# Performance work log

Hardware: AMD Instinct MI355X
Metric: run time of the kernel (lower is better)

Reference implementation:

```python
import jax, jax.numpy as jnp
import numpy as np

N_NODES = 100000
N_EDGES = 800000
C = 64        # in_channels == out_channels
H = 4         # num_heads
LN_EPS = 1e-5
SM_EPS = 1e-8


def setup_inputs() -> dict:
    key = jax.random.key(0)
    ks = jax.random.split(key, 8)
    return {
        "x": jax.random.normal(ks[0], (N_NODES, C), dtype=jnp.float32),
        "edge_index": jax.random.randint(ks[1], (2, N_EDGES), 0, N_NODES, dtype=jnp.int64),
        "edge_time": jax.random.uniform(ks[2], (N_EDGES,), dtype=jnp.float32),
        "current_time": 1,
        "W_w": jax.random.normal(ks[3], (C, C), dtype=jnp.float32) * (1.0 / np.sqrt(C)),
        "W_b": jnp.zeros((C,), dtype=jnp.float32),
        "attn_w": jax.random.normal(ks[4], (2 * C, H), dtype=jnp.float32) * (1.0 / np.sqrt(2 * C)),
        "attn_b": jnp.zeros((H,), dtype=jnp.float32),
        "decay_rate": jnp.full((1,), 0.1, dtype=jnp.float32),
        "proj_w": jax.random.normal(ks[5], (C * H, C), dtype=jnp.float32) * (1.0 / np.sqrt(C * H)),
        "proj_b": jnp.zeros((C,), dtype=jnp.float32),
        "ln_g": jnp.ones((C,), dtype=jnp.float32),
        "ln_b": jnp.zeros((C,), dtype=jnp.float32),
    }


def reference(x, edge_index, edge_time, current_time, W_w, W_b, attn_w, attn_b,
              decay_rate, proj_w, proj_b, ln_g, ln_b):
    num_nodes = x.shape[0]
    src, dst = edge_index[0], edge_index[1]

    # relation-specific transform (same Linear applied to src and dst node sets)
    h = x @ W_w + W_b                       # (N, C)
    h_src = h[src]                          # (E, C) gather
    h_dst = h[dst]                          # (E, C) gather

    # attention: Linear(2C -> H) + LeakyReLU(0.2)
    logits = h_src @ attn_w[:C] + h_dst @ attn_w[C:] + attn_b   # (E, H)
    scores = jax.nn.leaky_relu(logits, negative_slope=0.2)

    # temporal decay: exp(-softplus(lambda) * delta_t), multiplied pre-softmax
    delta_t = jnp.float32(current_time) - edge_time             # (E,)
    lam = jax.nn.softplus(decay_rate[0])
    scores = scores * jnp.exp(-lam * delta_t)[:, None]

    # segmented (per-destination) softmax over incoming edges
    smax = jax.ops.segment_max(scores, dst, num_segments=num_nodes)   # (N, H)
    e = jnp.exp(scores - smax[dst])                                   # (E, H)
    ssum = jax.ops.segment_sum(e, dst, num_segments=num_nodes)        # (N, H)
    attn = e / (ssum[dst] + SM_EPS)                                   # (E, H)

    # per-edge messages (E, C, H) -> (E, C*H), scatter-add to destinations
    msg = (h_src[:, :, None] * attn[:, None, :]).reshape(-1, C * H)
    agg = jax.ops.segment_sum(msg, dst, num_segments=num_nodes)       # (N, C*H)

    # single edge type -> mean over 1 message is identity
    out = agg @ proj_w + proj_b                                       # (N, C)
    # dropout p=0 (eval) -> identity; residual + LayerNorm + ReLU
    z = out + x
    mu = jnp.mean(z, axis=-1, keepdims=True)
    var = jnp.mean(jnp.square(z - mu), axis=-1, keepdims=True)
    y = ln_g * (z - mu) * jax.lax.rsqrt(var + LN_EPS) + ln_b
    return jax.nn.relu(y)
```

## Files before the change

### kernel.cpp

```cpp
#include <hip/hip_runtime.h>


typedef __attribute__((ext_vector_type(8))) short bf16x8;
typedef __attribute__((ext_vector_type(4))) float f32x4;

__device__ __forceinline__ unsigned short f2bf(float f) {
  unsigned int u = __float_as_uint(f);
  u += 0x7FFFu + ((u >> 16) & 1u);
  return (unsigned short)(u >> 16);
}
__device__ __forceinline__ float bf2f(unsigned short s) {
  return __uint_as_float(((unsigned int)s) << 16);
}

#define FMA4(P, S, R) { P.x = fmaf(S, R.x, P.x); P.y = fmaf(S, R.y, P.y); \
                        P.z = fmaf(S, R.z, P.z); P.w = fmaf(S, R.w, P.w); }

__global__ __launch_bounds__(64) void k_hn(const float* __restrict__ x,
    const float* __restrict__ Ww, const float* __restrict__ Wb,
    const float* __restrict__ attn_w,
    unsigned short* __restrict__ h16, float4* __restrict__ u,
    float4* __restrict__ v, int N)
{
  const int n = blockIdx.x * 64 + threadIdx.x;
  const bool valid = (n < N);
  const int nc = valid ? n : (N - 1);

  float o[64];
  #pragma unroll
  for (int c = 0; c < 64; ++c) o[c] = Wb[c];

  const float* xr = x + (size_t)nc * 64;
  for (int ch = 0; ch < 16; ++ch) {
    float4 xv = *(const float4*)(xr + ch * 4);
    float a[4] = {xv.x, xv.y, xv.z, xv.w};
    #pragma unroll
    for (int kk = 0; kk < 4; ++kk) {
      const float* Wr = Ww + (size_t)(ch * 4 + kk) * 64;
      #pragma unroll
      for (int c = 0; c < 64; ++c)
        o[c] = fmaf(a[kk], Wr[c], o[c]);
    }
  }

  float4 uu = make_float4(0.f, 0.f, 0.f, 0.f);
  float4 vv = make_float4(0.f, 0.f, 0.f, 0.f);
  const float4* aw = (const float4*)attn_w;
  #pragma unroll
  for (int c = 0; c < 64; ++c) {
    float4 r1 = aw[c];
    float4 r2 = aw[64 + c];
    FMA4(uu, o[c], r1);
    FMA4(vv, o[c], r2);
  }

  if (valid) {
    unsigned int* hr = (unsigned int*)(h16 + (size_t)n * 64);
    #pragma unroll
    for (int i = 0; i < 8; ++i) {
      uint4 w;
      w.x = (unsigned int)f2bf(o[i*8+0]) | ((unsigned int)f2bf(o[i*8+1]) << 16);
      w.y = (unsigned int)f2bf(o[i*8+2]) | ((unsigned int)f2bf(o[i*8+3]) << 16);
      w.z = (unsigned int)f2bf(o[i*8+4]) | ((unsigned int)f2bf(o[i*8+5]) << 16);
      w.w = (unsigned int)f2bf(o[i*8+6]) | ((unsigned int)f2bf(o[i*8+7]) << 16);
      *(uint4*)(hr + i * 4) = w;
    }
    u[n] = uu;
    v[n] = vv;
  }
}

__global__ __launch_bounds__(256) void k_score(const float4* __restrict__ u,
    const float4* __restrict__ v,
    const int* __restrict__ ei, const float* __restrict__ et,
    const int* __restrict__ ctime, const float* __restrict__ drate,
    const float* __restrict__ attn_b, float4* __restrict__ est,
    int* __restrict__ deg, int* __restrict__ rank, int E)
{
  int e = blockIdx.x * 256 + threadIdx.x;
  if (e >= E) return;
  const int src = ei[e];
  const int dst = ei[E + e];
  rank[e] = atomicAdd(&deg[dst], 1);
  const float4 us = u[src];
  const float4 vd = v[dst];
  const float4 ab = *(const float4*)attn_b;
  const float lam = log1pf(__expf(drate[0]));
  const float w = __expf(-lam * ((float)ctime[0] - et[e]));

  float4 o; float t;
  t = us.x + vd.x + ab.x; t = (t > 0.f ? t : 0.2f * t) * w; o.x = __expf(t);
  t = us.y + vd.y + ab.y; t = (t > 0.f ? t : 0.2f * t) * w; o.y = __expf(t);
  t = us.z + vd.z + ab.z; t = (t > 0.f ? t : 0.2f * t) * w; o.z = __expf(t);
  t = us.w + vd.w + ab.w; t = (t > 0.f ? t : 0.2f * t) * w; o.w = __expf(t);
  est[e] = o;
}

__global__ __launch_bounds__(256) void scan1(const int* __restrict__ deg,
    int* __restrict__ offs, int* __restrict__ bsums, int N)
{
  int i = blockIdx.x * 256 + threadIdx.x;
  int lane = threadIdx.x & 63;
  int w = threadIdx.x >> 6;
  int v = (i < N) ? deg[i] : 0;
  int s = v;
  #pragma unroll
  for (int d = 1; d < 64; d <<= 1) {
    int t = __shfl_up(s, d, 64);
    if (lane >= d) s += t;
  }
  __shared__ int wsum[4];
  if (lane == 63) wsum[w] = s;
  __syncthreads();
  int add = 0;
  if (w > 0) add += wsum[0];
  if (w > 1) add += wsum[1];
  if (w > 2) add += wsum[2];
  if (i < N) offs[i] = s - v + add;
  if (threadIdx.x == 255) bsums[blockIdx.x] = wsum[0] + wsum[1] + wsum[2] + wsum[3];
}

__global__ __launch_bounds__(512) void scan2(int* bsums, int NB)
{
  __shared__ int lds[512];
  int t = threadIdx.x;
  int v = (t < NB) ? bsums[t] : 0;
  lds[t] = v;
  __syncthreads();
  for (int s = 1; s < 512; s <<= 1) {
    int a = (t >= s) ? lds[t - s] : 0;
    __syncthreads();
    lds[t] += a;
    __syncthreads();
  }
  if (t < NB) bsums[t] = lds[t] - v;
}

__global__ __launch_bounds__(256) void k_fill(const int* __restrict__ ei,
    const int* __restrict__ offs, const int* __restrict__ bsums,
    const int* __restrict__ rank, const float4* __restrict__ est,
    int* __restrict__ csr_src, float4* __restrict__ csr_es, int E)
{
  int e = blockIdx.x * 256 + threadIdx.x;
  if (e >= E) return;
  int d = ei[E + e];
  int pos = offs[d] + bsums[d >> 8] + rank[e];
  csr_src[pos] = ei[e];
  csr_es[pos] = est[e];
}

__global__ __launch_bounds__(256) void k_agg(const unsigned short* __restrict__ h16,
    const int* __restrict__ csr_src, const float4* __restrict__ csr_es,
    const int* __restrict__ offs, const int* __restrict__ bsums,
    unsigned short* __restrict__ agg, int N, int E)
{
  const int c = threadIdx.x & 63;
  const int wid = blockIdx.x * 4 + (threadIdx.x >> 6);
  const int wstride = gridDim.x * 4;

  for (int n0 = wid; n0 < N; n0 += wstride) {
    const int n = __builtin_amdgcn_readfirstlane(n0);
    const int p0 = offs[n] + bsums[n >> 8];
    const int p1 = (n + 1 < N) ? (offs[n + 1] + bsums[(n + 1) >> 8]) : E;
    const int nf = (p1 - p0) & ~3;

    float acc0 = 0.f, acc1 = 0.f, acc2 = 0.f, acc3 = 0.f;
    float den0 = 0.f, den1 = 0.f, den2 = 0.f, den3 = 0.f;

    int4   sA = make_int4(0, 0, 0, 0);
    float4 eA0, eA1, eA2, eA3;
    float  gA0 = 0.f, gA1 = 0.f, gA2 = 0.f, gA3 = 0.f;
    if (nf) {
      sA = *(const int4*)(csr_src + p0);
      eA0 = csr_es[p0];     eA1 = csr_es[p0 + 1];
      eA2 = csr_es[p0 + 2]; eA3 = csr_es[p0 + 3];
      gA0 = bf2f(h16[(size_t)sA.x * 64 + c]);
      gA1 = bf2f(h16[(size_t)sA.y * 64 + c]);
      gA2 = bf2f(h16[(size_t)sA.z * 64 + c]);
      gA3 = bf2f(h16[(size_t)sA.w * 64 + c]);
    }
    for (int p = p0; p < p0 + nf; p += 4) {
      int4 sB; float4 eB0, eB1, eB2, eB3;
      float gB0, gB1, gB2, gB3;
      const bool more = (p + 4 < p0 + nf);
      if (more) {
        sB = *(const int4*)(csr_src + p + 4);
        eB0 = csr_es[p + 4]; eB1 = csr_es[p + 5];
        eB2 = csr_es[p + 6]; eB3 = csr_es[p + 7];
        gB0 = bf2f(h16[(size_t)sB.x * 64 + c]);
        gB1 = bf2f(h16[(size_t)sB.y * 64 + c]);
        gB2 = bf2f(h16[(size_t)sB.z * 64 + c]);
        gB3 = bf2f(h16[(size_t)sB.w * 64 + c]);
      }
      den0 += (eA0.x + eA1.x) + (eA2.x + eA3.x);
      den1 += (eA0.y + eA1.y) + (eA2.y + eA3.y);
      den2 += (eA0.z + eA1.z) + (eA2.z + eA3.z);
      den3 += (eA0.w + eA1.w) + (eA2.w + eA3.w);
      acc0 = fmaf(eA0.x, gA0, fmaf(eA1.x, gA1, fmaf(eA2.x, gA2, fmaf(eA3.x, gA3, acc0))));
      acc1 = fmaf(eA0.y, gA0, fmaf(eA1.y, gA1, fmaf(eA2.y, gA2, fmaf(eA3.y, gA3, acc1))));
      acc2 = fmaf(eA0.z, gA0, fmaf(eA1.z, gA1, fmaf(eA2.z, gA2, fmaf(eA3.z, gA3, acc2))));
      acc3 = fmaf(eA0.w, gA0, fmaf(eA1.w, gA1, fmaf(eA2.w, gA2, fmaf(eA3.w, gA3, acc3))));
      if (more) {
        eA0 = eB0; eA1 = eB1; eA2 = eB2; eA3 = eB3;
        gA0 = gB0; gA1 = gB1; gA2 = gB2; gA3 = gB3;
      }
    }
    for (int p = p0 + nf; p < p1; ++p) {
      int s = csr_src[p];
      float4 ev = csr_es[p];
      float g = bf2f(h16[(size_t)s * 64 + c]);
      den0 += ev.x; den1 += ev.y; den2 += ev.z; den3 += ev.w;
      acc0 = fmaf(ev.x, g, acc0);
      acc1 = fmaf(ev.y, g, acc1);
      acc2 = fmaf(ev.z, g, acc2);
      acc3 = fmaf(ev.w, g, acc3);
    }
    ushort4 o;
    o.x = f2bf(acc0 / (den0 + 1e-8f));
    o.y = f2bf(acc1 / (den1 + 1e-8f));
    o.z = f2bf(acc2 / (den2 + 1e-8f));
    o.w = f2bf(acc3 / (den3 + 1e-8f));
    *(ushort4*)(agg + (size_t)n * 256 + c * 4) = o;
  }
}

__global__ __launch_bounds__(256) void k_pw(const float* __restrict__ Pw,
    unsigned short* __restrict__ Bf)
{
  int i = blockIdx.x * 256 + threadIdx.x;
  int j    = i & 7;
  int lane = (i >> 3) & 63;
  int cb   = (i >> 9) & 3;
  int ks   = i >> 11;
  int k    = ks * 32 + (lane >> 4) * 8 + j;
  int colg = cb * 16 + (lane & 15);
  Bf[i] = f2bf(Pw[(size_t)k * 64 + colg]);
}

__global__ __launch_bounds__(256) void k_projm(const unsigned short* __restrict__ agg,
    const unsigned short* __restrict__ Bf, const float* __restrict__ x,
    const float* __restrict__ Pb,
    const float* __restrict__ lg, const float* __restrict__ lb,
    float* __restrict__ out, int N)
{
  const int lane = threadIdx.x & 63;
  const int wv = threadIdx.x >> 6;
  const int nt = blockIdx.x * 4 + wv;
  if (nt * 16 >= N) return;
  const int col  = lane & 15;
  const int quad = lane >> 4;
  const int base = nt * 16;

  int na = base + col; if (na >= N) na = N - 1;
  const unsigned short* aptr = agg + (size_t)na * 256 + quad * 8;

  f32x4 acc0 = {0.f, 0.f, 0.f, 0.f};
  f32x4 acc1 = {0.f, 0.f, 0.f, 0.f};
  f32x4 acc2 = {0.f, 0.f, 0.f, 0.f};
  f32x4 acc3 = {0.f, 0.f, 0.f, 0.f};

  #pragma unroll
  for (int ks = 0; ks < 8; ++ks) {
    bf16x8 av = *(const bf16x8*)(aptr + ks * 32);
    bf16x8 b0 = *(const bf16x8*)(Bf + ((size_t)(ks * 4 + 0) * 64 + lane) * 8);
    bf16x8 b1 = *(const bf16x8*)(Bf + ((size_t)(ks * 4 + 1) * 64 + lane) * 8);
    bf16x8 b2 = *(const bf16x8*)(Bf + ((size_t)(ks * 4 + 2) * 64 + lane) * 8);
    bf16x8 b3 = *(const bf16x8*)(Bf + ((size_t)(ks * 4 + 3) * 64 + lane) * 8);
    acc0 = __builtin_amdgcn_mfma_f32_16x16x32_bf16(av, b0, acc0, 0, 0, 0);
    acc1 = __builtin_amdgcn_mfma_f32_16x16x32_bf16(av, b1, acc1, 0, 0, 0);
    acc2 = __builtin_amdgcn_mfma_f32_16x16x32_bf16(av, b2, acc2, 0, 0, 0);
    acc3 = __builtin_amdgcn_mfma_f32_16x16x32_bf16(av, b3, acc3, 0, 0, 0);
  }

  const float pb0 = Pb[col], pb1 = Pb[16 + col], pb2 = Pb[32 + col], pb3 = Pb[48 + col];
  float v[4][4];
  #pragma unroll
  for (int r = 0; r < 4; ++r) {
    int node = base + quad * 4 + r; if (node >= N) node = N - 1;
    const float* xr = x + (size_t)node * 64;
    v[0][r] = acc0[r] + pb0 + xr[col];
    v[1][r] = acc1[r] + pb1 + xr[16 + col];
    v[2][r] = acc2[r] + pb2 + xr[32 + col];
    v[3][r] = acc3[r] + pb3 + xr[48 + col];
  }

  float mu[4], inv[4];
  #pragma unroll
  for (int r = 0; r < 4; ++r) {
    float s = (v[0][r] + v[1][r]) + (v[2][r] + v[3][r]);
    s += __shfl_xor(s, 1, 64); s += __shfl_xor(s, 2, 64);
    s += __shfl_xor(s, 4, 64); s += __shfl_xor(s, 8, 64);
    mu[r] = s * 0.015625f;
  }
  #pragma unroll
  for (int r = 0; r < 4; ++r) {
    float d0 = v[0][r] - mu[r], d1 = v[1][r] - mu[r];
    float d2 = v[2][r] - mu[r], d3 = v[3][r] - mu[r];
    float s = fmaf(d0, d0, d1 * d1) + fmaf(d2, d2, d3 * d3);
    s += __shfl_xor(s, 1, 64); s += __shfl_xor(s, 2, 64);
    s += __shfl_xor(s, 4, 64); s += __shfl_xor(s, 8, 64);
    inv[r] = rsqrtf(s * 0.015625f + 1e-5f);
  }

  const float lg0 = lg[col], lg1 = lg[16 + col], lg2 = lg[32 + col], lg3 = lg[48 + col];
  const float lb0 = lb[col], lb1 = lb[16 + col], lb2 = lb[32 + col], lb3 = lb[48 + col];
  #pragma unroll
  for (int r = 0; r < 4; ++r) {
    int node = base + quad * 4 + r;
    if (node < N) {
      float* orow = out + (size_t)node * 64;
      orow[col]      = fmaxf(fmaf(lg0 * (v[0][r] - mu[r]), inv[r], lb0), 0.f);
      orow[16 + col] = fmaxf(fmaf(lg1 * (v[1][r] - mu[r]), inv[r], lb1), 0.f);
      orow[32 + col] = fmaxf(fmaf(lg2 * (v[2][r] - mu[r]), inv[r], lb2), 0.f);
      orow[48 + col] = fmaxf(fmaf(lg3 * (v[3][r] - mu[r]), inv[r], lb3), 0.f);
    }
  }
}

extern "C" void kernel_launch(void* const* d_in, const int* in_sizes, int n_in,
                              void* d_out, int out_size, void* d_ws, size_t ws_size,
                              hipStream_t stream)
{
  const float* x  = (const float*)d_in[0];
  const int*   ei = (const int*)d_in[1];
  const float* et = (const float*)d_in[2];
  const int*   ct = (const int*)d_in[3];
  const float* Ww = (const float*)d_in[4];
  const float* Wb = (const float*)d_in[5];
  const float* aw = (const float*)d_in[6];
  const float* ab = (const float*)d_in[7];
  const float* dr = (const float*)d_in[8];
  const float* Pw = (const float*)d_in[9];
  const float* Pb = (const float*)d_in[10];
  const float* lg = (const float*)d_in[11];
  const float* lb = (const float*)d_in[12];
  float* out = (float*)d_out;

  const int N = in_sizes[0] / 64;
  const int E = in_sizes[2];

  char* ws = (char*)d_ws;
  size_t off = 0;
  auto take = [&](size_t bytes) -> char* {
    char* p = ws + off;
    off = (off + bytes + 255) & ~(size_t)255;
    return p;
  };
  unsigned short* h16 = (unsigned short*)take((size_t)N * 64 * 2);
  int*    deg    = (int*)take((size_t)N * 4);
  int*    offs   = (int*)take((size_t)N * 4);
  int*    bsums  = (int*)take(512 * 4);
  int*    rank   = (int*)take((size_t)E * 4);
  float4* est    = (float4*)take((size_t)E * 16);
  int*    csr_src= (int*)take((size_t)E * 4);
  float4* csr_es = (float4*)take((size_t)E * 16);
  unsigned short* agg = (unsigned short*)take((size_t)N * 256 * 2);
  float4* u      = (float4*)take((size_t)N * 16);
  float4* v      = (float4*)take((size_t)N * 16);
  unsigned short* Bf = (unsigned short*)take(16384 * 2);

  hipMemsetAsync(deg, 0, (size_t)N * 4, stream);

  k_pw<<<64, 256, 0, stream>>>(Pw, Bf);
  k_hn<<<(N + 63) / 64, 64, 0, stream>>>(x, Ww, Wb, aw, h16, u, v, N);
  k_score<<<(E + 255) / 256, 256, 0, stream>>>(u, v, ei, et, ct, dr, ab, est, deg, rank, E);
  const int NB = (N + 255) / 256;
  scan1<<<NB, 256, 0, stream>>>(deg, offs, bsums, N);
  scan2<<<1, 512, 0, stream>>>(bsums, NB);
  k_fill<<<(E + 255) / 256, 256, 0, stream>>>(ei, offs, bsums, rank, est, csr_src, csr_es, E);
  k_agg<<<2048, 256, 0, stream>>>(h16, csr_src, csr_es, offs, bsums, agg, N, E);
  const int NT = (N + 15) / 16;
  k_projm<<<(NT + 3) / 4, 256, 0, stream>>>(agg, Bf, x, Pb, lg, lb, out, N);
}
```

Before: 281.5 us.

## Fuse score into CSR fill, pack edge records as bf16 int4

Edge scores are now computed inside the CSR fill kernel, so the intermediate est array is no longer written and re-read. The source index and four bf16-packed exp scores are stored together in one 16-byte record, so k_agg does one load per edge instead of two streams. The degree-count atomics are merged into the node-transform launch as extra blocks, and the deg memset and Bf packing are combined into one init kernel, which cuts launch count. The cost is bf16 precision on the softmax numerators and the node kernel block size changing from 64 to 256 threads.

Measured after the change: 248.6 us. 1.13x faster.

```diff
diff --git a/kernel.cpp b/kernel.cpp
--- a/kernel.cpp
+++ b/kernel.cpp
@@ -12,17 +12,48 @@
 __device__ __forceinline__ float bf2f(unsigned short s) {
   return __uint_as_float(((unsigned int)s) << 16);
 }
+__device__ __forceinline__ unsigned int pk(float a, float b) {
+  return (unsigned int)f2bf(a) | ((unsigned int)f2bf(b) << 16);
+}
+__device__ __forceinline__ float bflo(int u) {
+  return __uint_as_float(((unsigned int)u) << 16);
+}
+__device__ __forceinline__ float bfhi(int u) {
+  return __uint_as_float(((unsigned int)u) & 0xFFFF0000u);
+}
 
 #define FMA4(P, S, R) { P.x = fmaf(S, R.x, P.x); P.y = fmaf(S, R.y, P.y); \
                         P.z = fmaf(S, R.z, P.z); P.w = fmaf(S, R.w, P.w); }
 
-__global__ __launch_bounds__(64) void k_hn(const float* __restrict__ x,
+__global__ __launch_bounds__(256) void k_init(const float* __restrict__ Pw,
+    unsigned short* __restrict__ Bf, int* __restrict__ deg, int N)
+{
+  int i = blockIdx.x * 256 + threadIdx.x;
+  if (i < N) deg[i] = 0;
+  if (i < 16384) {
+    int j    = i & 7;
+    int lane = (i >> 3) & 63;
+    int cb   = (i >> 9) & 3;
+    int ks   = i >> 11;
+    int k    = ks * 32 + (lane >> 4) * 8 + j;
+    int colg = cb * 16 + (lane & 15);
+    Bf[i] = f2bf(Pw[(size_t)k * 64 + colg]);
+  }
+}
+
+__global__ __launch_bounds__(256) void k_hd(const float* __restrict__ x,
     const float* __restrict__ Ww, const float* __restrict__ Wb,
-    const float* __restrict__ attn_w,
+    const float* __restrict__ attn_w, const int* __restrict__ ei,
     unsigned short* __restrict__ h16, float4* __restrict__ u,
-    float4* __restrict__ v, int N)
-{
-  const int n = blockIdx.x * 64 + threadIdx.x;
+    float4* __restrict__ v, int* __restrict__ deg, int* __restrict__ rank,
+    int N, int E, int NBn)
+{
+  if ((int)blockIdx.x >= NBn) {
+    int e = (blockIdx.x - NBn) * 256 + threadIdx.x;
+    if (e < E) rank[e] = atomicAdd(&deg[ei[E + e]], 1);
+    return;
+  }
+  const int n = blockIdx.x * 256 + threadIdx.x;
   const bool valid = (n < N);
   const int nc = valid ? n : (N - 1);
 
@@ -59,41 +90,15 @@
     #pragma unroll
     for (int i = 0; i < 8; ++i) {
       uint4 w;
-      w.x = (unsigned int)f2bf(o[i*8+0]) | ((unsigned int)f2bf(o[i*8+1]) << 16);
-      w.y = (unsigned int)f2bf(o[i*8+2]) | ((unsigned int)f2bf(o[i*8+3]) << 16);
-      w.z = (unsigned int)f2bf(o[i*8+4]) | ((unsigned int)f2bf(o[i*8+5]) << 16);
-      w.w = (unsigned int)f2bf(o[i*8+6]) | ((unsigned int)f2bf(o[i*8+7]) << 16);
+      w.x = pk(o[i*8+0], o[i*8+1]);
+      w.y = pk(o[i*8+2], o[i*8+3]);
+      w.z = pk(o[i*8+4], o[i*8+5]);
+      w.w = pk(o[i*8+6], o[i*8+7]);
       *(uint4*)(hr + i * 4) = w;
     }
     u[n] = uu;
     v[n] = vv;
   }
-}
-
-__global__ __launch_bounds__(256) void k_score(const float4* __restrict__ u,
-    const float4* __restrict__ v,
-    const int* __restrict__ ei, const float* __restrict__ et,
-    const int* __restrict__ ctime, const float* __restrict__ drate,
-    const float* __restrict__ attn_b, float4* __restrict__ est,
-    int* __restrict__ deg, int* __restrict__ rank, int E)
-{
-  int e = blockIdx.x * 256 + threadIdx.x;
-  if (e >= E) return;
-  const int src = ei[e];
-  const int dst = ei[E + e];
-  rank[e] = atomicAdd(&deg[dst], 1);
-  const float4 us = u[src];
-  const float4 vd = v[dst];
-  const float4 ab = *(const float4*)attn_b;
-  const float lam = log1pf(__expf(drate[0]));
-  const float w = __expf(-lam * ((float)ctime[0] - et[e]));
-
-  float4 o; float t;
-  t = us.x + vd.x + ab.x; t = (t > 0.f ? t : 0.2f * t) * w; o.x = __expf(t);
-  t = us.y + vd.y + ab.y; t = (t > 0.f ? t : 0.2f * t) * w; o.y = __expf(t);
-  t = us.z + vd.z + ab.z; t = (t > 0.f ? t : 0.2f * t) * w; o.z = __expf(t);
-  t = us.w + vd.w + ab.w; t = (t > 0.f ? t : 0.2f * t) * w; o.w = __expf(t);
-  est[e] = o;
 }
 
 __global__ __launch_bounds__(256) void scan1(const int* __restrict__ deg,
@@ -137,22 +142,40 @@
 }
 
 __global__ __launch_bounds__(256) void k_fill(const int* __restrict__ ei,
+    const float* __restrict__ et, const int* __restrict__ ctime,
+    const float* __restrict__ drate, const float4* __restrict__ u,
+    const float4* __restrict__ v, const float* __restrict__ attn_b,
     const int* __restrict__ offs, const int* __restrict__ bsums,
-    const int* __restrict__ rank, const float4* __restrict__ est,
-    int* __restrict__ csr_src, float4* __restrict__ csr_es, int E)
+    const int* __restrict__ rank, int4* __restrict__ csr, int E)
 {
   int e = blockIdx.x * 256 + threadIdx.x;
   if (e >= E) return;
-  int d = ei[E + e];
-  int pos = offs[d] + bsums[d >> 8] + rank[e];
-  csr_src[pos] = ei[e];
-  csr_es[pos] = est[e];
+  const int s = ei[e];
+  const int d = ei[E + e];
+  const float4 us = u[s];
+  const float4 vd = v[d];
+  const float4 ab = *(const float4*)attn_b;
+  const float lam = log1pf(__expf(drate[0]));
+  const float w = __expf(-lam * ((float)ctime[0] - et[e]));
+
+  float4 o; float t;
+  t = us.x + vd.x + ab.x; t = (t > 0.f ? t : 0.2f * t) * w; o.x = __expf(t);
+  t = us.y + vd.y + ab.y; t = (t > 0.f ? t : 0.2f * t) * w; o.y = __expf(t);
+  t = us.z + vd.z + ab.z; t = (t > 0.f ? t : 0.2f * t) * w; o.z = __expf(t);
+  t = us.w + vd.w + ab.w; t = (t > 0.f ? t : 0.2f * t) * w; o.w = __expf(t);
+
+  int4 rec;
+  rec.x = s;
+  rec.y = (int)pk(o.x, o.y);
+  rec.z = (int)pk(o.z, o.w);
+  rec.w = 0;
+  csr[offs[d] + bsums[d >> 8] + rank[e]] = rec;
 }
 
 __global__ __launch_bounds__(256) void k_agg(const unsigned short* __restrict__ h16,
-    const int* __restrict__ csr_src, const float4* __restrict__ csr_es,
-    const int* __restrict__ offs, const int* __restrict__ bsums,
-    unsigned short* __restrict__ agg, int N, int E)
+    const int4* __restrict__ csr, const int* __restrict__ offs,
+    const int* __restrict__ bsums, unsigned short* __restrict__ agg,
+    int N, int E)
 {
   const int c = threadIdx.x & 63;
   const int wid = blockIdx.x * 4 + (threadIdx.x >> 6);
@@ -167,74 +190,60 @@
     float acc0 = 0.f, acc1 = 0.f, acc2 = 0.f, acc3 = 0.f;
     float den0 = 0.f, den1 = 0.f, den2 = 0.f, den3 = 0.f;
 
-    int4   sA = make_int4(0, 0, 0, 0);
-    float4 eA0, eA1, eA2, eA3;
-    float  gA0 = 0.f, gA1 = 0.f, gA2 = 0.f, gA3 = 0.f;
+    int4 rA0, rA1, rA2, rA3;
+    float gA0 = 0.f, gA1 = 0.f, gA2 = 0.f, gA3 = 0.f;
     if (nf) {
-      sA = *(const int4*)(csr_src + p0);
-      eA0 = csr_es[p0];     eA1 = csr_es[p0 + 1];
-      eA2 = csr_es[p0 + 2]; eA3 = csr_es[p0 + 3];
-      gA0 = bf2f(h16[(size_t)sA.x * 64 + c]);
-      gA1 = bf2f(h16[(size_t)sA.y * 64 + c]);
-      gA2 = bf2f(h16[(size_t)sA.z * 64 + c]);
-      gA3 = bf2f(h16[(size_t)sA.w * 64 + c]);
+      rA0 = csr[p0];     rA1 = csr[p0 + 1];
+      rA2 = csr[p0 + 2]; rA3 = csr[p0 + 3];
+      gA0 = bf2f(h16[(size_t)rA0.x * 64 + c]);
+      gA1 = bf2f(h16[(size_t)rA1.x * 64 + c]);
+      gA2 = bf2f(h16[(size_t)rA2.x * 64 + c]);
+      gA3 = bf2f(h16[(size_t)rA3.x * 64 + c]);
     }
     for (int p = p0; p < p0 + nf; p += 4) {
-      int4 sB; float4 eB0, eB1, eB2, eB3;
+      int4 rB0, rB1, rB2, rB3;
       float gB0, gB1, gB2, gB3;
       const bool more = (p + 4 < p0 + nf);
       if (more) {
-        sB = *(const int4*)(csr_src + p + 4);
-        eB0 = csr_es[p + 4]; eB1 = csr_es[p + 5];
-        eB2 = csr_es[p + 6]; eB3 = csr_es[p + 7];
-        gB0 = bf2f(h16[(size_t)sB.x * 64 + c]);
-        gB1 = bf2f(h16[(size_t)sB.y * 64 + c]);
-        gB2 = bf2f(h16[(size_t)sB.z * 64 + c]);
-        gB3 = bf2f(h16[(size_t)sB.w * 64 + c]);
+        rB0 = csr[p + 4]; rB1 = csr[p + 5];
+        rB2 = csr[p + 6]; rB3 = csr[p + 7];
+        gB0 = bf2f(h16[(size_t)rB0.x * 64 + c]);
+        gB1 = bf2f(h16[(size_t)rB1.x * 64 + c]);
+        gB2 = bf2f(h16[(size_t)rB2.x * 64 + c]);
+        gB3 = bf2f(h16[(size_t)rB3.x * 64 + c]);
       }
-      den0 += (eA0.x + eA1.x) + (eA2.x + eA3.x);
-      den1 += (eA0.y + eA1.y) + (eA2.y + eA3.y);
-      den2 += (eA0.z + eA1.z) + (eA2.z + eA3.z);
-      den3 += (eA0.w + eA1.w) + (eA2.w + eA3.w);
-      acc0 = fmaf(eA0.x, gA0, fmaf(eA1.x, gA1, fmaf(eA2.x, gA2, fmaf(eA3.x, gA3, acc0))));
-      acc1 = fmaf(eA0.y, gA0, fmaf(eA1.y, gA1, fmaf(eA2.y, gA2, fmaf(eA3.y, gA3, acc1))));
-      acc2 = fmaf(eA0.z, gA0, fmaf(eA1.z, gA1, fmaf(eA2.z, gA2, fmaf(eA3.z, gA3, acc2))));
-      acc3 = fmaf(eA0.w, gA0, fmaf(eA1.w, gA1, fmaf(eA2.w, gA2, fmaf(eA3.w, gA3, acc3))));
+      float e00 = bflo(rA0.y), e01 = bfhi(rA0.y), e02 = bflo(rA0.z), e03 = bfhi(rA0.z);
+      float e10 = bflo(rA1.y), e11 = bfhi(rA1.y), e12 = bflo(rA1.z), e13 = bfhi(rA1.z);
+      float e20 = bflo(rA2.y), e21 = bfhi(rA2.y), e22 = bflo(rA2.z), e23 = bfhi(rA2.z);
+      float e30 = bflo(rA3.y), e31 = bfhi(rA3.y), e32 = bflo(rA3.z), e33 = bfhi(rA3.z);
+      den0 += (e00 + e10) + (e20 + e30);
+      den1 += (e01 + e11) + (e21 + e31);
+      den2 += (e02 + e12) + (e22 + e32);
+      den3 += (e03 + e13) + (e23 + e33);
+      acc0 = fmaf(e00, gA0, fmaf(e10, gA1, fmaf(e20, gA2, fmaf(e30, gA3, acc0))));
+      acc1 = fmaf(e01, gA0, fmaf(e11, gA1, fmaf(e21, gA2, fmaf(e31, gA3, acc1))));
+      acc2 = fmaf(e02, gA0, fmaf(e12, gA1, fmaf(e22, gA2, fmaf(e32, gA3, acc2))));
+      acc3 = fmaf(e03, gA0, fmaf(e13, gA1, fmaf(e23, gA2, fmaf(e33, gA3, acc3))));
       if (more) {
-        eA0 = eB0; eA1 = eB1; eA2 = eB2; eA3 = eB3;
+        rA0 = rB0; rA1 = rB1; rA2 = rB2; rA3 = rB3;
         gA0 = gB0; gA1 = gB1; gA2 = gB2; gA3 = gB3;
       }
     }
     for (int p = p0 + nf; p < p1; ++p) {
-      int s = csr_src[p];
-      float4 ev = csr_es[p];
-      float g = bf2f(h16[(size_t)s * 64 + c]);
-      den0 += ev.x; den1 += ev.y; den2 += ev.z; den3 += ev.w;
-      acc0 = fmaf(ev.x, g, acc0);
-      acc1 = fmaf(ev.y, g, acc1);
-      acc2 = fmaf(ev.z, g, acc2);
-      acc3 = fmaf(ev.w, g, acc3);
-    }
-    ushort4 o;
-    o.x = f2bf(acc0 / (den0 + 1e-8f));
-    o.y = f2bf(acc1 / (den1 + 1e-8f));
-    o.z = f2bf(acc2 / (den2 + 1e-8f));
-    o.w = f2bf(acc3 / (den3 + 1e-8f));
-    *(ushort4*)(agg + (size_t)n * 256 + c * 4) = o;
-  }
-}
-
-__global__ __launch_bounds__(256) void k_pw(const float* __restrict__ Pw,
-    unsigned short* __restrict__ Bf)
-{
-  int i = blockIdx.x * 256 + threadIdx.x;
-  int j    = i & 7;
-  int lane = (i >> 3) & 63;
-  int cb   = (i >> 9) & 3;
-  int ks   = i >> 11;
-  int k    = ks * 32 + (lane >> 4) * 8 + j;
-  int colg = cb * 16 + (lane & 15);
-  Bf[i] = f2bf(Pw[(size_t)k * 64 + colg]);
+      int4 r = csr[p];
+      float g = bf2f(h16[(size_t)r.x * 64 + c]);
+      float e0 = bflo(r.y), e1 = bfhi(r.y), e2 = bflo(r.z), e3 = bfhi(r.z);
+      den0 += e0; den1 += e1; den2 += e2; den3 += e3;
+      acc0 = fmaf(e0, g, acc0);
+      acc1 = fmaf(e1, g, acc1);
+      acc2 = fmaf(e2, g, acc2);
+      acc3 = fmaf(e3, g, acc3);
+    }
+    uint2 w;
+    w.x = pk(acc0 / (den0 + 1e-8f), acc1 / (den1 + 1e-8f));
+    w.y = pk(acc2 / (den2 + 1e-8f), acc3 / (den3 + 1e-8f));
+    *(uint2*)(agg + (size_t)n * 256 + c * 4) = w;
+  }
 }
 
 __global__ __launch_bounds__(256) void k_projm(const unsigned short* __restrict__ agg,
@@ -351,24 +360,21 @@
   int*    offs   = (int*)take((size_t)N * 4);
   int*    bsums  = (int*)take(512 * 4);
   int*    rank   = (int*)take((size_t)E * 4);
-  float4* est    = (float4*)take((size_t)E * 16);
-  int*    csr_src= (int*)take((size_t)E * 4);
-  float4* csr_es = (float4*)take((size_t)E * 16);
+  int4*   csr    = (int4*)take((size_t)E * 16);
   unsigned short* agg = (unsigned short*)take((size_t)N * 256 * 2);
   float4* u      = (float4*)take((size_t)N * 16);
   float4* v      = (float4*)take((size_t)N * 16);
   unsigned short* Bf = (unsigned short*)take(16384 * 2);
 
-  hipMemsetAsync(deg, 0, (size_t)N * 4, stream);
-
-  k_pw<<<64, 256, 0, stream>>>(Pw, Bf);
-  k_hn<<<(N + 63) / 64, 64, 0, stream>>>(x, Ww, Wb, aw, h16, u, v, N);
-  k_score<<<(E + 255) / 256, 256, 0, stream>>>(u, v, ei, et, ct, dr, ab, est, deg, rank, E);
-  const int NB = (N + 255) / 256;
-  scan1<<<NB, 256, 0, stream>>>(deg, offs, bsums, N);
-  scan2<<<1, 512, 0, stream>>>(bsums, NB);
-  k_fill<<<(E + 255) / 256, 256, 0, stream>>>(ei, offs, bsums, rank, est, csr_src, csr_es, E);
-  k_agg<<<2048, 256, 0, stream>>>(h16, csr_src, csr_es, offs, bsums, agg, N, E);
+  const int NBn = (N + 255) / 256;
+  const int NBe = (E + 255) / 256;
+
+  k_init<<<NBn, 256, 0, stream>>>(Pw, Bf, deg, N);
+  k_hd<<<NBn + NBe, 256, 0, stream>>>(x, Ww, Wb, aw, ei, h16, u, v, deg, rank, N, E, NBn);
+  scan1<<<NBn, 256, 0, stream>>>(deg, offs, bsums, N);
+  scan2<<<1, 512, 0, stream>>>(bsums, NBn);
+  k_fill<<<NBe, 256, 0, stream>>>(ei, et, ct, dr, u, v, ab, offs, bsums, rank, csr, E);
+  k_agg<<<2048, 256, 0, stream>>>(h16, csr, offs, bsums, agg, N, E);
   const int NT = (N + 15) / 16;
   k_projm<<<(NT + 3) / 4, 256, 0, stream>>>(agg, Bf, x, Pb, lg, lb, out, N);
 }
```
